# Performance work log

Hardware: AMD Instinct MI355X
Metric: run time of the kernel (lower is better)

Reference implementation:

```python
import jax, jax.numpy as jnp
import numpy as np

B = 16384
STATE = 524   # state_dim / output_size
IENC = 256    # INet output dim
ZD = 32       # z_dim
H = 256       # expert hidden size
E = 5         # num_experts
HG = 256      # gating hidden size
IN1 = STATE + IENC + ZD   # 812, PredictionNet layer-1 input
IN2 = H + ZD              # 288, layers 2/3 input


def _uni(k, shape):
    # matches PredictionNet.init_params glorot-style uniform bound
    bound = float(np.sqrt(6.0 / (shape[-2] * shape[-1])))
    return jax.random.uniform(k, shape, jnp.float32, -bound, bound)


def setup_inputs() -> dict:
    key = jax.random.key(0)
    ks = jax.random.split(key, 12)
    d = {}
    d['z'] = jax.random.normal(ks[0], (B, ZD), jnp.float32)
    d['p_prev'] = jax.random.normal(ks[1], (B, STATE), jnp.float32)
    d['I'] = jax.random.normal(ks[2], (B, 2048), jnp.float32)
    # gating network: (state+z) -> HG -> HG//2 -> E
    d['gw1'] = _uni(ks[3], (STATE + ZD, HG)); d['gb1'] = jnp.zeros((HG,), jnp.float32)
    d['gw2'] = _uni(ks[4], (HG, HG // 2));    d['gb2'] = jnp.zeros((HG // 2,), jnp.float32)
    d['gw3'] = _uni(ks[5], (HG // 2, E));     d['gb3'] = jnp.zeros((E,), jnp.float32)
    # INet: 2048 -> 256 -> 256 -> 256
    d['iw1'] = _uni(ks[6], (2048, IENC)); d['ib1'] = jnp.zeros((IENC,), jnp.float32)
    d['iw2'] = _uni(ks[7], (IENC, IENC)); d['ib2'] = jnp.zeros((IENC,), jnp.float32)
    d['iw3'] = _uni(ks[8], (IENC, IENC)); d['ib3'] = jnp.zeros((IENC,), jnp.float32)
    # expert weights [E, in, out], biases [E, out]
    d['w_l1'] = _uni(ks[9], (E, IN1, H));     d['b_l1'] = jnp.zeros((E, H), jnp.float32)
    d['w_l2'] = _uni(ks[10], (E, IN2, H));    d['b_l2'] = jnp.zeros((E, H), jnp.float32)
    d['w_l3'] = _uni(ks[11], (E, IN2, STATE)); d['b_l3'] = jnp.zeros((E, STATE), jnp.float32)
    return d


def reference(z, p_prev, I, gw1, gb1, gw2, gb2, gw3, gb3,
              iw1, ib1, iw2, ib2, iw3, ib3,
              w_l1, b_l1, w_l2, b_l2, w_l3, b_l3):
    elu = jax.nn.elu
    # gating network -> softmax blending coefficients omega [B, E]
    g = elu(jnp.concatenate([z, p_prev], axis=1) @ gw1 + gb1)
    g = elu(g @ gw2 + gb2)
    omega = jax.nn.softmax(g @ gw3 + gb3, axis=-1)
    # interaction encoder
    Ienc = elu(elu(elu(I @ iw1 + ib1) @ iw2 + ib2) @ iw3 + ib3)
    x = jnp.concatenate([p_prev, Ienc], axis=1)  # [B, STATE+IENC]

    def moe_linear(h, W, b):
        # same math as sum_e omega_e * (h @ W_e) + omega @ b, without
        # materializing per-sample blended [B, in, out] weights
        per_expert = jnp.einsum('bi,eio->beo', h, W)
        return jnp.einsum('be,beo->bo', omega, per_expert) + omega @ b

    h0 = jnp.concatenate([z, x], axis=1)          # [B, 812]
    h1 = elu(moe_linear(h0, w_l1, b_l1))          # [B, 256]
    h2 = elu(moe_linear(jnp.concatenate([z, h1], axis=1), w_l2, b_l2))
    h3 = moe_linear(jnp.concatenate([z, h2], axis=1), w_l3, b_l3)  # [B, 524]
    return h3
```

## Files before the change

kernel.cpp:

```cpp
#include <hip/hip_runtime.h>
#include <hip/hip_bf16.h>
#include <cstdint>
#include <cstddef>


#define BATCH 16384

typedef __attribute__((ext_vector_type(8))) short short8;
typedef __attribute__((ext_vector_type(4))) float f32x4;
typedef unsigned short u16;
typedef unsigned int u32;

typedef __attribute__((address_space(3))) void lds_t;
typedef __attribute__((address_space(1))) void gmem_t;

__device__ __forceinline__ void gload16(const u16* g, u16* l) {
  __builtin_amdgcn_global_load_lds((gmem_t*)(u16*)g, (lds_t*)l, 16, 0, 0);
}

__device__ __forceinline__ float bf2f(u16 u) {
  union { float f; u32 i; } v; v.i = ((u32)u) << 16; return v.f;
}
__device__ __forceinline__ u16 f2bf(float f) {
  union { float f; u32 i; } v; v.f = f;
  u32 x = v.i;
  return (u16)((x + 0x7fffu + ((x >> 16) & 1u)) >> 16);
}
__device__ __forceinline__ u16 load_bf(const void* p, long i, int f32) {
  return f32 ? f2bf(((const float*)p)[i]) : ((const u16*)p)[i];
}
__device__ __forceinline__ float elu_f(float x) { return x > 0.f ? x : expm1f(x); }

__device__ __forceinline__ int swz(int row, int q) { return q ^ ((row >> 1) & 3); }

__global__ __launch_bounds__(256) void detect_dtype(const u32* __restrict__ zr,
                                                    int* __restrict__ flag)
{
  __shared__ int cnt;
  if (threadIdx.x == 0) cnt = 0;
  __syncthreads();
  u32 w = zr[threadIdx.x];
  int e = (w >> 7) & 0xFF;
  if (e >= 112 && e <= 142) atomicAdd(&cnt, 1);
  __syncthreads();
  if (threadIdx.x == 0) *flag = (cnt < 128) ? 1 : 0;
}

__global__ __launch_bounds__(256) void prep_kernel(
    const void* __restrict__ z, const void* __restrict__ p,
    const int* __restrict__ flagp,
    u16* __restrict__ h0, u16* __restrict__ h1c, u16* __restrict__ h2c,
    const void* ib1, const void* ib2, const void* ib3,
    const void* gb1, const void* gb2, const void* gb3,
    const void* gw3, const void* bl1, const void* bl2, const void* bl3,
    u16* __restrict__ smallc)
{
  const int f32 = *flagp;
  const int b = blockIdx.y;
  const int c = blockIdx.x * 256 + threadIdx.x;
  if (blockIdx.y == 0 && blockIdx.x == 0) {
    for (long j = threadIdx.x; j < 7100; j += 256) {
      u16 v;
      if      (j < 256)  v = load_bf(ib1, j,        f32);
      else if (j < 512)  v = load_bf(ib2, j - 256,  f32);
      else if (j < 768)  v = load_bf(ib3, j - 512,  f32);
      else if (j < 1024) v = load_bf(gb1, j - 768,  f32);
      else if (j < 1152) v = load_bf(gb2, j - 1024, f32);
      else if (j < 1280) v = (j - 1152 < 5) ? load_bf(gb3, j - 1152, f32) : (u16)0;
      else if (j < 1920) v = load_bf(gw3, j - 1280, f32);
      else if (j < 3200) v = load_bf(bl1, j - 1920, f32);
      else if (j < 4480) v = load_bf(bl2, j - 3200, f32);
      else               v = load_bf(bl3, j - 4480, f32);
      smallc[j] = v;
    }
  }
  if (c >= 832) return;
  const long i = (long)b * 832 + c;
  if (c < 32) {
    u16 v = load_bf(z, (long)b * 32 + c, f32);
    h0[i] = v;
    h1c[(long)b * 288 + c] = v;
    h2c[(long)b * 288 + c] = v;
  } else if (c < 556) {
    h0[i] = load_bf(p, (long)b * 524 + (c - 32), f32);
  } else if (c >= 812) {
    h0[i] = 0;
  }
}

__global__ __launch_bounds__(256) void convert_I(
    const void* __restrict__ I, const int* __restrict__ flagp,
    u16* __restrict__ out)
{
  const int f32 = *flagp;
  const long total8 = (long)BATCH * 2048 / 8;
  const long stride = (long)gridDim.x * blockDim.x;
  for (long t = (long)blockIdx.x * blockDim.x + threadIdx.x; t < total8; t += stride) {
    if (f32) {
      const float4* src = (const float4*)I;
      float4 a = src[t * 2], b = src[t * 2 + 1];
      union { u16 r[8]; uint4 v; } u;
      u.r[0] = f2bf(a.x); u.r[1] = f2bf(a.y); u.r[2] = f2bf(a.z); u.r[3] = f2bf(a.w);
      u.r[4] = f2bf(b.x); u.r[5] = f2bf(b.y); u.r[6] = f2bf(b.z); u.r[7] = f2bf(b.w);
      *(uint4*)(out + t * 8) = u.v;
    } else {
      *(uint4*)(out + t * 8) = ((const uint4*)I)[t];
    }
  }
}

struct TPSeg { long end; int K, N, Kp, Np; };

__global__ __launch_bounds__(256) void transpose_all(
    const int* __restrict__ flagp,
    const void* s0, const void* s1, const void* s2, const void* s3,
    const void* s4, const void* s5, const void* s6, const void* s7,
    u16* d0, u16* d1, u16* d2, u16* d3, u16* d4, u16* d5, u16* d6, u16* d7)
{
  const TPSeg seg[8] = {
    {  524288, 2048, 256, 2048, 256 },
    {  589824,  256, 256,  256, 256 },
    {  655360,  256, 256,  256, 256 },
    {  802816,  556, 256,  576, 256 },
    {  835584,  256, 128,  256, 128 },
    { 1900544,  812, 256,  832, 256 },
    { 2269184,  288, 256,  288, 256 },
    { 3098624,  288, 524,  288, 576 },
  };
  const void* const srcs[8] = { s0, s1, s2, s3, s4, s5, s6, s7 };
  u16* const dsts[8] = { d0, d1, d2, d3, d4, d5, d6, d7 };
  const int f32 = *flagp;
  const long total = 3098624;
  const long stride = (long)gridDim.x * blockDim.x;
  for (long i = (long)blockIdx.x * blockDim.x + threadIdx.x; i < total; i += stride) {
    int s = 0;
    long base = 0;
    while (i >= seg[s].end) { base = seg[s].end; ++s; }
    const long j = i - base;
    const int Kp = seg[s].Kp, Np = seg[s].Np, K = seg[s].K, N = seg[s].N;
    const int k = (int)(j % Kp);
    const long t = j / Kp;
    const int n = (int)(t % Np);
    const int e = (int)(t / Np);
    u16 v = 0;
    if (k < K && n < N) v = load_bf(srcs[s], (long)e * K * N + (long)k * N + n, f32);
    dsts[s][j] = v;
  }
}

template<bool ELU>
__global__ __launch_bounds__(256, 2) void gemm64(
    const u16* __restrict__ A, int lda,
    const u16* __restrict__ Wt, int ldw,
    const u16* __restrict__ bias,
    u16* __restrict__ C, int ldc, int col_off, int K)
{
  __shared__ __align__(16) u16 sA[2][64 * 32];
  __shared__ __align__(16) u16 sB[2][128 * 32];

  const int tid  = threadIdx.x;
  const int bm   = blockIdx.x, bn = blockIdx.y;
  const int lane = tid & 63, wave = tid >> 6;
  const int wm = (wave & 1) * 32, wn = (wave >> 1) * 64;
  const int lrow = lane & 15, lq = lane >> 4;

  const int sq    = (lane & 3) ^ ((lane >> 3) & 3);
  const int srowA = 16 * wave + (lane >> 2);
  const int srowB = 32 * wave + (lane >> 2);
  const u16* Ag = A  + (size_t)(bm * 64  + srowA) * lda + sq * 8;
  const u16* Wg = Wt + (size_t)(bn * 128 + srowB) * ldw + sq * 8;
  const int laOff = wave * 512;
  const int lbOff = wave * 1024;

  f32x4 acc[2][4] = {};
  const int nt = K / 32;

  gload16(Ag, sA[0] + laOff);
  gload16(Wg, sB[0] + lbOff);
  gload16(Wg + (size_t)16 * ldw, sB[0] + lbOff + 512);
  __syncthreads();

  for (int t = 0; t < nt; ++t) {
    const int cur = t & 1;
    if (t + 1 < nt) {
      const int k0 = (t + 1) * 32;
      gload16(Ag + k0, sA[cur ^ 1] + laOff);
      gload16(Wg + k0, sB[cur ^ 1] + lbOff);
      gload16(Wg + (size_t)16 * ldw + k0, sB[cur ^ 1] + lbOff + 512);
    }

    short8 a[2], b[4];
#pragma unroll
    for (int i = 0; i < 2; ++i) {
      const int r = wm + i * 16 + lrow;
      a[i] = *(const short8*)(sA[cur] + r * 32 + swz(r, lq) * 8);
    }
#pragma unroll
    for (int i = 0; i < 4; ++i) {
      const int r = wn + i * 16 + lrow;
      b[i] = *(const short8*)(sB[cur] + r * 32 + swz(r, lq) * 8);
    }

#pragma unroll
    for (int mi = 0; mi < 2; ++mi)
#pragma unroll
      for (int ni = 0; ni < 4; ++ni)
        acc[mi][ni] = __builtin_amdgcn_mfma_f32_16x16x32_bf16(a[mi], b[ni], acc[mi][ni], 0, 0, 0);

    __syncthreads();
  }

#pragma unroll
  for (int ni = 0; ni < 4; ++ni) {
    const int col = bn * 128 + wn + ni * 16 + lrow;
    const float bv = bf2f(bias[col]);
#pragma unroll
    for (int mi = 0; mi < 2; ++mi) {
#pragma unroll
      for (int r = 0; r < 4; ++r) {
        const int row = bm * 64 + wm + mi * 16 + lq * 4 + r;
        float v = acc[mi][ni][r] + bv;
        if (ELU) v = elu_f(v);
        C[(size_t)row * ldc + col_off + col] = f2bf(v);
      }
    }
  }
}

__global__ __launch_bounds__(256) void gating3_kernel(
    const u16* __restrict__ g2, const u16* __restrict__ gw3c,
    const u16* __restrict__ gb3c, float* __restrict__ omega)
{
  const int wid  = (blockIdx.x << 2) + (threadIdx.x >> 6);
  const int lane = threadIdx.x & 63;
  const u32 gp = *(const u32*)(g2 + (size_t)wid * 128 + lane * 2);
  const float x0 = bf2f((u16)(gp & 0xffffu));
  const float x1 = bf2f((u16)(gp >> 16));
  float acc[5];
#pragma unroll
  for (int e = 0; e < 5; ++e)
    acc[e] = x0 * bf2f(gw3c[(lane * 2) * 5 + e]) + x1 * bf2f(gw3c[(lane * 2 + 1) * 5 + e]);
#pragma unroll
  for (int off = 1; off < 64; off <<= 1) {
#pragma unroll
    for (int e = 0; e < 5; ++e) acc[e] += __shfl_xor(acc[e], off);
  }
  if (lane == 0) {
    float t[5], m = -1e30f;
#pragma unroll
    for (int e = 0; e < 5; ++e) { t[e] = acc[e] + bf2f(gb3c[e]); m = fmaxf(m, t[e]); }
    float s = 0.f;
#pragma unroll
    for (int e = 0; e < 5; ++e) { t[e] = expf(t[e] - m); s += t[e]; }
    const float inv = 1.f / s;
#pragma unroll
    for (int e = 0; e < 5; ++e) omega[(size_t)wid * 5 + e] = t[e] * inv;
  }
}

template<bool ELU>
__global__ __launch_bounds__(256, 2) void moe_gemm(
    const u16* __restrict__ A, int lda,
    const u16* __restrict__ Wt, int ldw, long wstride_e,
    const u16* __restrict__ bias, int bias_n,
    const float* __restrict__ omega,
    void* __restrict__ C, int ldc, int col_off, int n_store, int K,
    const int* __restrict__ flagp, int is_final)
{
  __shared__ __align__(16) u16 sA[2][128 * 32];
  __shared__ __align__(16) u16 sW[2][5][64 * 32];
  __shared__ float som[128 * 5];
  __shared__ float sbias[5][64];

  const int tid  = threadIdx.x;
  const int bm   = blockIdx.x, bn = blockIdx.y;
  const int lane = tid & 63, wave = tid >> 6;
  const int wm = (wave & 1) * 64, wn = (wave >> 1) * 32;
  const int lrow = lane & 15, lq = lane >> 4;
  const int f32out = is_final ? *flagp : 0;

  const int sq = (lane & 3) ^ ((lane >> 3) & 3);
  const int srowA = 32 * wave + (lane >> 2);
  const int srowW = 16 * wave + (lane >> 2);
  const u16* Ag = A  + (size_t)(bm * 128 + srowA) * lda + sq * 8;
  const u16* Wg = Wt + (size_t)(bn * 64 + srowW) * ldw + sq * 8;
  const int laOff = wave * 1024;
  const int lWoff = wave * 512;

  f32x4 acc[5][4][2] = {};
  const int nt = K / 32;

  gload16(Ag, sA[0] + laOff);
  gload16(Ag + (size_t)16 * lda, sA[0] + laOff + 512);
#pragma unroll
  for (int e = 0; e < 5; ++e)
    gload16(Wg + e * wstride_e, sW[0][e] + lWoff);

  for (int t = tid; t < 960; t += 256) {
    if (t < 640) {
      som[t] = omega[(size_t)(bm * 128) * 5 + t];
    } else {
      const int j = t - 640;
      const int e = j >> 6, c = j & 63;
      const int col = bn * 64 + c;
      sbias[e][c] = (col < bias_n) ? bf2f(bias[(size_t)e * bias_n + col]) : 0.f;
    }
  }
  __syncthreads();

  for (int t = 0; t < nt; ++t) {
    const int cur = t & 1;
    if (t + 1 < nt) {
      const int k0 = (t + 1) * 32;
      gload16(Ag + k0, sA[cur ^ 1] + laOff);
      gload16(Ag + (size_t)16 * lda + k0, sA[cur ^ 1] + laOff + 512);
#pragma unroll
      for (int e = 0; e < 5; ++e)
        gload16(Wg + e * wstride_e + k0, sW[cur ^ 1][e] + lWoff);
    }

    short8 a[4];
#pragma unroll
    for (int i = 0; i < 4; ++i) {
      const int r = wm + i * 16 + lrow;
      a[i] = *(const short8*)(sA[cur] + r * 32 + swz(r, lq) * 8);
    }
    const int rb0 = wn + lrow, rb1 = rb0 + 16;
    const int ob0 = rb0 * 32 + swz(rb0, lq) * 8;
    const int ob1 = rb1 * 32 + swz(rb1, lq) * 8;
#pragma unroll
    for (int e = 0; e < 5; ++e) {
      short8 b0 = *(const short8*)(sW[cur][e] + ob0);
      short8 b1 = *(const short8*)(sW[cur][e] + ob1);
#pragma unroll
      for (int mi = 0; mi < 4; ++mi) {
        acc[e][mi][0] = __builtin_amdgcn_mfma_f32_16x16x32_bf16(a[mi], b0, acc[e][mi][0], 0, 0, 0);
        acc[e][mi][1] = __builtin_amdgcn_mfma_f32_16x16x32_bf16(a[mi], b1, acc[e][mi][1], 0, 0, 0);
      }
    }

    __syncthreads();
  }

#pragma unroll
  for (int mi = 0; mi < 4; ++mi) {
#pragma unroll
    for (int r = 0; r < 4; ++r) {
      const int rl = wm + mi * 16 + lq * 4 + r;
      const int row = bm * 128 + rl;
      float om[5];
#pragma unroll
      for (int e = 0; e < 5; ++e) om[e] = som[rl * 5 + e];
#pragma unroll
      for (int ni = 0; ni < 2; ++ni) {
        const int c = wn + ni * 16 + lrow;
        const int col = bn * 64 + c;
        if (col < n_store) {
          float v = 0.f;
#pragma unroll
          for (int e = 0; e < 5; ++e) v += om[e] * (acc[e][mi][ni][r] + sbias[e][c]);
          if (ELU) v = elu_f(v);
          const size_t idx = (size_t)row * ldc + col_off + col;
          if (f32out) ((float*)C)[idx] = v;
          else        ((u16*)C)[idx]   = f2bf(v);
        }
      }
    }
  }
}

extern "C" void kernel_launch(void* const* d_in, const int* in_sizes, int n_in,
                              void* d_out, int out_size, void* d_ws, size_t ws_size,
                              hipStream_t stream)
{
  const void* z    = d_in[0];
  const void* pprev= d_in[1];
  const void* I    = d_in[2];
  const void* gw1  = d_in[3];
  const void* gb1  = d_in[4];
  const void* gw2  = d_in[5];
  const void* gb2  = d_in[6];
  const void* gw3  = d_in[7];
  const void* gb3  = d_in[8];
  const void* iw1  = d_in[9];
  const void* ib1  = d_in[10];
  const void* iw2  = d_in[11];
  const void* ib2  = d_in[12];
  const void* iw3  = d_in[13];
  const void* ib3  = d_in[14];
  const void* wl1  = d_in[15];
  const void* bl1  = d_in[16];
  const void* wl2  = d_in[17];
  const void* bl2  = d_in[18];
  const void* wl3  = d_in[19];
  const void* bl3  = d_in[20];

  char* base = (char*)d_ws;
  size_t off = 0;
  auto alloc = [&](size_t bytes) -> void* {
    void* p = base + off;
    off = (off + bytes + 255) & ~(size_t)255;
    return p;
  };

  const size_t B = BATCH;
  int* flagp   = (int*)alloc(256);
  u16* h0      = (u16*)alloc(B * 832 * 2);
  u16* h1c     = (u16*)alloc(B * 288 * 2);
  u16* h2c     = (u16*)alloc(B * 288 * 2);
  u16* i1      = (u16*)alloc(B * 256 * 2);
  u16* i2      = (u16*)alloc(B * 256 * 2);
  float* omega = (float*)alloc(B * 5 * 4);
  u16* Ibf     = (u16*)alloc(B * 2048 * 2);
  u16* smallc  = (u16*)alloc(7100 * 2);
  u16* iw1t = (u16*)alloc((size_t)256 * 2048 * 2);
  u16* iw2t = (u16*)alloc((size_t)256 * 256 * 2);
  u16* iw3t = (u16*)alloc((size_t)256 * 256 * 2);
  u16* gw1t = (u16*)alloc((size_t)256 * 576 * 2);
  u16* gw2t = (u16*)alloc((size_t)128 * 256 * 2);
  u16* wl1t = (u16*)alloc((size_t)5 * 256 * 832 * 2);
  u16* wl2t = (u16*)alloc((size_t)5 * 256 * 288 * 2);
  u16* wl3t = (u16*)alloc((size_t)5 * 576 * 288 * 2);
  u16* g1 = i1;
  u16* g2 = i2;
  (void)in_sizes; (void)n_in; (void)out_size; (void)ws_size;

  u16* ib1c = smallc + 0,   *ib2c = smallc + 256, *ib3c = smallc + 512;
  u16* gb1c = smallc + 768, *gb2c = smallc + 1024, *gb3c = smallc + 1152;
  u16* gw3c = smallc + 1280;
  u16* bl1c = smallc + 1920, *bl2c = smallc + 3200, *bl3c = smallc + 4480;

  detect_dtype<<<1, 256, 0, stream>>>((const u32*)z, flagp);
  prep_kernel<<<dim3(4, BATCH), 256, 0, stream>>>(z, pprev, flagp, h0, h1c, h2c,
      ib1, ib2, ib3, gb1, gb2, gb3, gw3, bl1, bl2, bl3, smallc);
  convert_I<<<4096, 256, 0, stream>>>(I, flagp, Ibf);
  transpose_all<<<3072, 256, 0, stream>>>(flagp,
      iw1, iw2, iw3, gw1, gw2, wl1, wl2, wl3,
      iw1t, iw2t, iw3t, gw1t, gw2t, wl1t, wl2t, wl3t);

  gemm64<true><<<dim3(BATCH/64, 2), 256, 0, stream>>>(Ibf, 2048, iw1t, 2048, ib1c, i1, 256, 0,   2048);
  gemm64<true><<<dim3(BATCH/64, 2), 256, 0, stream>>>(i1,  256,  iw2t, 256,  ib2c, i2, 256, 0,   256);
  gemm64<true><<<dim3(BATCH/64, 2), 256, 0, stream>>>(i2,  256,  iw3t, 256,  ib3c, h0, 832, 556, 256);

  gemm64<true><<<dim3(BATCH/64, 2), 256, 0, stream>>>(h0, 832, gw1t, 576, gb1c, g1, 256, 0, 576);
  gemm64<true><<<dim3(BATCH/64, 1), 256, 0, stream>>>(g1, 256, gw2t, 256, gb2c, g2, 128, 0, 256);
  gating3_kernel<<<BATCH/4, 256, 0, stream>>>(g2, gw3c, gb3c, omega);

  moe_gemm<true><<<dim3(BATCH/128, 4), 256, 0, stream>>>(
      h0, 832, wl1t, 832, (long)256 * 832, bl1c, 256, omega, h1c, 288, 32, 256, 832, flagp, 0);
  moe_gemm<true><<<dim3(BATCH/128, 4), 256, 0, stream>>>(
      h1c, 288, wl2t, 288, (long)256 * 288, bl2c, 256, omega, h2c, 288, 32, 256, 288, flagp, 0);
  moe_gemm<false><<<dim3(BATCH/128, 9), 256, 0, stream>>>(
      h2c, 288, wl3t, 288, (long)576 * 288, bl3c, 524, omega, d_out, 524, 0, 524, 288, flagp, 1);
}
```

Measured before the change: 557.9 us.

## Triple-buffer GEMM pipelines and enlarge MoE tiles to 256 rows with split loader waves

Both GEMM kernels move from double to triple buffering, with prefetch two steps ahead. Each k-step now syncs through explicit vmcnt waits and raw s_barrier calls instead of __syncthreads, and setprio is raised around the MFMA block. The MoE GEMM grows to 512 threads and 256-row tiles. In that kernel four waves load A and four waves load the five expert weight slices, which halves redundant weight reloads per batch row. The cost is more LDS per block, which may reduce occupancy, and the hand-counted vmcnt values must match the number of loads issued for correctness.

```diff
diff --git a/kernel.cpp b/kernel.cpp
--- a/kernel.cpp
+++ b/kernel.cpp
@@ -16,6 +16,12 @@
 
 __device__ __forceinline__ void gload16(const u16* g, u16* l) {
   __builtin_amdgcn_global_load_lds((gmem_t*)(u16*)g, (lds_t*)l, 16, 0, 0);
+}
+
+__device__ __forceinline__ void barrier_nodrain() {
+  asm volatile("" ::: "memory");
+  __builtin_amdgcn_s_barrier();
+  asm volatile("" ::: "memory");
 }
 
 __device__ __forceinline__ float bf2f(u16 u) {
@@ -155,8 +161,8 @@
     const u16* __restrict__ bias,
     u16* __restrict__ C, int ldc, int col_off, int K)
 {
-  __shared__ __align__(16) u16 sA[2][64 * 32];
-  __shared__ __align__(16) u16 sB[2][128 * 32];
+  __shared__ __align__(16) u16 sA[3][64 * 32];
+  __shared__ __align__(16) u16 sB[3][128 * 32];
 
   const int tid  = threadIdx.x;
   const int bm   = blockIdx.x, bn = blockIdx.y;
@@ -178,16 +184,26 @@
   gload16(Ag, sA[0] + laOff);
   gload16(Wg, sB[0] + lbOff);
   gload16(Wg + (size_t)16 * ldw, sB[0] + lbOff + 512);
+  gload16(Ag + 32, sA[1] + laOff);
+  gload16(Wg + 32, sB[1] + lbOff);
+  gload16(Wg + (size_t)16 * ldw + 32, sB[1] + lbOff + 512);
   __syncthreads();
 
   for (int t = 0; t < nt; ++t) {
-    const int cur = t & 1;
-    if (t + 1 < nt) {
-      const int k0 = (t + 1) * 32;
-      gload16(Ag + k0, sA[cur ^ 1] + laOff);
-      gload16(Wg + k0, sB[cur ^ 1] + lbOff);
-      gload16(Wg + (size_t)16 * ldw + k0, sB[cur ^ 1] + lbOff + 512);
-    }
+    const int cur = t % 3;
+    barrier_nodrain();
+    if (t + 2 < nt) {
+      const int nb = (t + 2) % 3;
+      const int k0 = (t + 2) * 32;
+      gload16(Ag + k0, sA[nb] + laOff);
+      gload16(Wg + k0, sB[nb] + lbOff);
+      gload16(Wg + (size_t)16 * ldw + k0, sB[nb] + lbOff + 512);
+    }
+    const int ahead = nt - 1 - t;
+    if (ahead >= 2)      asm volatile("s_waitcnt vmcnt(6)" ::: "memory");
+    else if (ahead == 1) asm volatile("s_waitcnt vmcnt(3)" ::: "memory");
+    else                 asm volatile("s_waitcnt vmcnt(0)" ::: "memory");
+    barrier_nodrain();
 
     short8 a[2], b[4];
 #pragma unroll
@@ -201,13 +217,13 @@
       b[i] = *(const short8*)(sB[cur] + r * 32 + swz(r, lq) * 8);
     }
 
+    __builtin_amdgcn_s_setprio(1);
 #pragma unroll
     for (int mi = 0; mi < 2; ++mi)
 #pragma unroll
       for (int ni = 0; ni < 4; ++ni)
         acc[mi][ni] = __builtin_amdgcn_mfma_f32_16x16x32_bf16(a[mi], b[ni], acc[mi][ni], 0, 0, 0);
-
-    __syncthreads();
+    __builtin_amdgcn_s_setprio(0);
   }
 
 #pragma unroll
@@ -259,7 +275,7 @@
 }
 
 template<bool ELU>
-__global__ __launch_bounds__(256, 2) void moe_gemm(
+__global__ __launch_bounds__(512, 2) void moe_gemm(
     const u16* __restrict__ A, int lda,
     const u16* __restrict__ Wt, int ldw, long wstride_e,
     const u16* __restrict__ bias, int bias_n,
@@ -267,40 +283,62 @@
     void* __restrict__ C, int ldc, int col_off, int n_store, int K,
     const int* __restrict__ flagp, int is_final)
 {
-  __shared__ __align__(16) u16 sA[2][128 * 32];
-  __shared__ __align__(16) u16 sW[2][5][64 * 32];
-  __shared__ float som[128 * 5];
+  __shared__ __align__(16) u16 sA[3][256 * 32];
+  __shared__ __align__(16) u16 sW[3][5 * 64 * 32];
+  __shared__ float som[256 * 5];
   __shared__ float sbias[5][64];
 
   const int tid  = threadIdx.x;
   const int bm   = blockIdx.x, bn = blockIdx.y;
   const int lane = tid & 63, wave = tid >> 6;
-  const int wm = (wave & 1) * 64, wn = (wave >> 1) * 32;
+  const int wm = (wave & 3) * 64, wn = (wave >> 2) * 32;
   const int lrow = lane & 15, lq = lane >> 4;
   const int f32out = is_final ? *flagp : 0;
 
   const int sq = (lane & 3) ^ ((lane >> 3) & 3);
-  const int srowA = 32 * wave + (lane >> 2);
-  const int srowW = 16 * wave + (lane >> 2);
-  const u16* Ag = A  + (size_t)(bm * 128 + srowA) * lda + sq * 8;
-  const u16* Wg = Wt + (size_t)(bn * 64 + srowW) * ldw + sq * 8;
-  const int laOff = wave * 1024;
-  const int lWoff = wave * 512;
+  const int isA = (wave < 4);
+
+  const u16* gp[5];
+  int ldst[5];
+  if (isA) {
+#pragma unroll
+    for (int j = 0; j < 4; ++j) {
+      const int row = 64 * wave + 16 * j + (lane >> 2);
+      gp[j] = A + (size_t)(bm * 256 + row) * lda + sq * 8;
+      ldst[j] = wave * 2048 + j * 512;
+    }
+    gp[4] = gp[0]; ldst[4] = ldst[0];
+  } else {
+#pragma unroll
+    for (int j = 0; j < 5; ++j) {
+      const int d = 5 * (wave - 4) + j;
+      const int e = d >> 2, s = d & 3;
+      const int row = 16 * s + (lane >> 2);
+      gp[j] = Wt + (size_t)e * wstride_e + (size_t)(bn * 64 + row) * ldw + sq * 8;
+      ldst[j] = d * 512;
+    }
+  }
+
+  auto stage = [&](int buf, int k0) {
+    if (isA) {
+#pragma unroll
+      for (int j = 0; j < 4; ++j) gload16(gp[j] + k0, sA[buf] + ldst[j]);
+    } else {
+#pragma unroll
+      for (int j = 0; j < 5; ++j) gload16(gp[j] + k0, sW[buf] + ldst[j]);
+    }
+  };
 
   f32x4 acc[5][4][2] = {};
   const int nt = K / 32;
 
-  gload16(Ag, sA[0] + laOff);
-  gload16(Ag + (size_t)16 * lda, sA[0] + laOff + 512);
-#pragma unroll
-  for (int e = 0; e < 5; ++e)
-    gload16(Wg + e * wstride_e, sW[0][e] + lWoff);
-
-  for (int t = tid; t < 960; t += 256) {
-    if (t < 640) {
-      som[t] = omega[(size_t)(bm * 128) * 5 + t];
+  stage(0, 0);
+  stage(1, 32);
+  for (int t2 = tid; t2 < 1600; t2 += 512) {
+    if (t2 < 1280) {
+      som[t2] = omega[(size_t)(bm * 256) * 5 + t2];
     } else {
-      const int j = t - 640;
+      const int j = t2 - 1280;
       const int e = j >> 6, c = j & 63;
       const int col = bn * 64 + c;
       sbias[e][c] = (col < bias_n) ? bf2f(bias[(size_t)e * bias_n + col]) : 0.f;
@@ -309,15 +347,20 @@
   __syncthreads();
 
   for (int t = 0; t < nt; ++t) {
-    const int cur = t & 1;
-    if (t + 1 < nt) {
-      const int k0 = (t + 1) * 32;
-      gload16(Ag + k0, sA[cur ^ 1] + laOff);
-      gload16(Ag + (size_t)16 * lda + k0, sA[cur ^ 1] + laOff + 512);
-#pragma unroll
-      for (int e = 0; e < 5; ++e)
-        gload16(Wg + e * wstride_e + k0, sW[cur ^ 1][e] + lWoff);
-    }
+    const int cur = t % 3;
+    barrier_nodrain();
+    if (t + 2 < nt) stage((t + 2) % 3, (t + 2) * 32);
+    const int ahead = nt - 1 - t;
+    if (isA) {
+      if (ahead >= 2)      asm volatile("s_waitcnt vmcnt(8)"  ::: "memory");
+      else if (ahead == 1) asm volatile("s_waitcnt vmcnt(4)"  ::: "memory");
+      else                 asm volatile("s_waitcnt vmcnt(0)"  ::: "memory");
+    } else {
+      if (ahead >= 2)      asm volatile("s_waitcnt vmcnt(10)" ::: "memory");
+      else if (ahead == 1) asm volatile("s_waitcnt vmcnt(5)"  ::: "memory");
+      else                 asm volatile("s_waitcnt vmcnt(0)"  ::: "memory");
+    }
+    barrier_nodrain();
 
     short8 a[4];
 #pragma unroll
@@ -328,18 +371,18 @@
     const int rb0 = wn + lrow, rb1 = rb0 + 16;
     const int ob0 = rb0 * 32 + swz(rb0, lq) * 8;
     const int ob1 = rb1 * 32 + swz(rb1, lq) * 8;
+    __builtin_amdgcn_s_setprio(1);
 #pragma unroll
     for (int e = 0; e < 5; ++e) {
-      short8 b0 = *(const short8*)(sW[cur][e] + ob0);
-      short8 b1 = *(const short8*)(sW[cur][e] + ob1);
+      short8 b0 = *(const short8*)(sW[cur] + e * 2048 + ob0);
+      short8 b1 = *(const short8*)(sW[cur] + e * 2048 + ob1);
 #pragma unroll
       for (int mi = 0; mi < 4; ++mi) {
         acc[e][mi][0] = __builtin_amdgcn_mfma_f32_16x16x32_bf16(a[mi], b0, acc[e][mi][0], 0, 0, 0);
         acc[e][mi][1] = __builtin_amdgcn_mfma_f32_16x16x32_bf16(a[mi], b1, acc[e][mi][1], 0, 0, 0);
       }
     }
-
-    __syncthreads();
+    __builtin_amdgcn_s_setprio(0);
   }
 
 #pragma unroll
@@ -347,7 +390,7 @@
 #pragma unroll
     for (int r = 0; r < 4; ++r) {
       const int rl = wm + mi * 16 + lq * 4 + r;
-      const int row = bm * 128 + rl;
+      const int row = bm * 256 + rl;
       float om[5];
 #pragma unroll
       for (int e = 0; e < 5; ++e) om[e] = som[rl * 5 + e];
@@ -446,10 +489,10 @@
   gemm64<true><<<dim3(BATCH/64, 1), 256, 0, stream>>>(g1, 256, gw2t, 256, gb2c, g2, 128, 0, 256);
   gating3_kernel<<<BATCH/4, 256, 0, stream>>>(g2, gw3c, gb3c, omega);
 
-  moe_gemm<true><<<dim3(BATCH/128, 4), 256, 0, stream>>>(
+  moe_gemm<true><<<dim3(BATCH/256, 4), 512, 0, stream>>>(
       h0, 832, wl1t, 832, (long)256 * 832, bl1c, 256, omega, h1c, 288, 32, 256, 832, flagp, 0);
-  moe_gemm<true><<<dim3(BATCH/128, 4), 256, 0, stream>>>(
+  moe_gemm<true><<<dim3(BATCH/256, 4), 512, 0, stream>>>(
       h1c, 288, wl2t, 288, (long)256 * 288, bl2c, 256, omega, h2c, 288, 32, 256, 288, flagp, 0);
-  moe_gemm<false><<<dim3(BATCH/128, 9), 256, 0, stream>>>(
+  moe_gemm<false><<<dim3(BATCH/256, 9), 512, 0, stream>>>(
       h2c, 288, wl3t, 288, (long)576 * 288, bl3c, 524, omega, d_out, 524, 0, 524, 288, flagp, 1);
 }
```

Result: slower. 602.1 us (+7.9%).
